# Optimization experiments

Measured on AMD Instinct MI355X. Metric: run time of the kernel, lower is better.

## Reference

```python
import jax, jax.numpy as jnp
import numpy as np
from jax import lax

# ---- module hyperparameters (from init_kwargs) ----
B = 8          # number of point clouds in the batch
NP = 4096      # points per cloud
C_IN = 64      # input feature channels
RATIO = 0.25   # fps ratio -> M_PER = 1024 centroids per cloud
R = 0.2        # ball-query radius
K = 64         # max_num_neighbors (hardcoded in the torch forward)
BIG = 1e10     # sentinel distance for out-of-radius pairs


def _fps(p, m):
    """Farthest point sampling on one cloud p:[Np,3] -> m local indices.
    Deterministic start at index 0 (torch_geometric uses a random start)."""
    mind = jnp.sum((p - p[0]) ** 2, axis=-1)  # [Np] dist^2 to first pick

    def step(mind, _):
        nxt = jnp.argmax(mind)
        d = jnp.sum((p - p[nxt]) ** 2, axis=-1)
        return jnp.minimum(mind, d), nxt

    _, rest = lax.scan(step, mind, None, length=m - 1)
    return jnp.concatenate([jnp.zeros((1,), rest.dtype), rest])  # [m]


def _ball_knn(p, s):
    """Radius query with neighbor cap: for each sampled point, the K nearest
    points within radius R (same cloud). p:[Np,3], s:[m] -> idx [m,K], mask [m,K].
    Note: every centroid contains itself (d=0), so each row has >=1 valid entry."""
    q = p[s]                                              # [m,3]
    d2 = jnp.sum((q[:, None, :] - p[None, :, :]) ** 2, axis=-1)  # [m,Np]
    dm = jnp.where(d2 <= R * R, d2, BIG)
    negv, idx = lax.top_k(-dm, K)                         # nearest-K within ball
    return idx, (-negv) < (BIG * 0.5)


def setup_inputs() -> dict:
    key = jax.random.key(0)
    k = jax.random.split(key, 6)
    x = jax.random.normal(k[0], (B * NP, C_IN), dtype=jnp.float32)
    pos = jax.random.uniform(k[1], (B * NP, 3), dtype=jnp.float32)  # unit cube
    batch = jnp.repeat(jnp.arange(B, dtype=jnp.int32), NP)

    def lin(kk, fi, fo):
        return jax.random.normal(kk, (fi, fo), dtype=jnp.float32) / np.float32(np.sqrt(fi))

    W1 = lin(k[2], C_IN + 3, 64); b1 = jnp.zeros((64,), jnp.float32)
    W2 = lin(k[3], 64, 64);       b2 = jnp.zeros((64,), jnp.float32)
    W3 = lin(k[4], 64, 128);      b3 = jnp.zeros((128,), jnp.float32)
    return dict(x=x, pos=pos, batch=batch, W1=W1, b1=b1, W2=W2, b2=b2,
                W3=W3, b3=b3, num_graphs=B)


def reference(x, pos, batch, W1, b1, W2, b2, W3, b3, num_graphs):
    Bn = int(num_graphs)
    N = pos.shape[0]
    Np = N // Bn
    m = int(Np * RATIO)

    posb = pos.reshape(Bn, Np, 3)
    sel = jax.vmap(lambda p: _fps(p, m))(posb)          # [B,m] local idx
    nbr, mask = jax.vmap(_ball_knn)(posb, sel)          # [B,m,K]

    offs = jnp.arange(Bn, dtype=sel.dtype) * Np
    sel_g = (sel + offs[:, None]).reshape(-1)           # [M] global centroid idx
    nbr_g = (nbr + offs[:, None, None]).reshape(Bn * m, K)
    maskf = mask.reshape(Bn * m, K)

    pos_s = pos[sel_g]                                  # [M,3]
    rel = pos[nbr_g] - pos_s[:, None, :]                # [M,K,3] pos_j - pos_i
    h = jnp.concatenate([x[nbr_g], rel], axis=-1)       # [M,K,C_IN+3]
    # PointNetConv local_nn (Linear-ReLU-Linear-ReLU-Linear), max aggregation
    h = jax.nn.relu(h @ W1 + b1)
    h = jax.nn.relu(h @ W2 + b2)
    h = h @ W3 + b3                                     # [M,K,128]
    h = jnp.where(maskf[:, :, None], h, jnp.float32(-1e30))
    x_out = jnp.max(h, axis=1)                          # [M,128]

    return x_out, pos_s, batch[sel_g]
```

## Files before the change

kernel.cpp:

```cpp
#include <hip/hip_runtime.h>
#include <math.h>

#define NB   8
#define NPTS 4096
#define MPER 1024
#define MTOT (NB*MPER)
#define CIN  64
#define KNN  64
#define CAP  512
#define R2D  0.04000000000000001

typedef unsigned int u32;
typedef unsigned long long u64;
using s16x8 = __attribute__((ext_vector_type(8))) short;
using f32x4 = __attribute__((ext_vector_type(4))) float;

__device__ __forceinline__ float d2f(float ax, float ay, float az,
                                     float bx, float by, float bz) {
    float dx = __fsub_rn(ax, bx);
    float dy = __fsub_rn(ay, by);
    float dz = __fsub_rn(az, bz);
    return __fadd_rn(__fadd_rn(__fmul_rn(dx, dx), __fmul_rn(dy, dy)),
                     __fmul_rn(dz, dz));
}

__device__ __forceinline__ unsigned short f2bf(float f) {
    u32 x = __float_as_uint(f);
    u32 r = (x + 0x7fffu + ((x >> 16) & 1u)) >> 16;
    return (unsigned short)r;
}
__device__ __forceinline__ u32 pk2(float a, float b) {
    return (u32)f2bf(a) | ((u32)f2bf(b) << 16);
}

__device__ __forceinline__ f32x4 mfma16(s16x8 a, s16x8 b, f32x4 c) {
    return __builtin_amdgcn_mfma_f32_16x16x32_bf16(a, b, c, 0, 0, 0);
}

__device__ __forceinline__ unsigned long long wave_max_u64_dpp(unsigned long long key)
{
#define DPPMAX(ctrl, rmask) do {                                                   \
        unsigned int lo_ = (unsigned int)key;                                      \
        unsigned int hi_ = (unsigned int)(key >> 32);                              \
        unsigned int plo = (unsigned int)__builtin_amdgcn_update_dpp(              \
            0, (int)lo_, ctrl, rmask, 0xf, false);                                 \
        unsigned int phi = (unsigned int)__builtin_amdgcn_update_dpp(              \
            0, (int)hi_, ctrl, rmask, 0xf, false);                                 \
        unsigned long long pk = ((unsigned long long)phi << 32) | plo;             \
        if (pk > key) key = pk;                                                    \
    } while (0)
    DPPMAX(0x111, 0xf);
    DPPMAX(0x112, 0xf);
    DPPMAX(0x114, 0xf);
    DPPMAX(0x118, 0xf);
    DPPMAX(0x142, 0xa);
    DPPMAX(0x143, 0xc);
#undef DPPMAX
    return key;
}

__global__ __launch_bounds__(256) void fps_kernel(const float* __restrict__ pos,
                                                  int* __restrict__ sel)
{
    const int b    = blockIdx.x;
    const int t    = threadIdx.x;
    const int lane = t & 63;
    const int wv   = t >> 6;
    const float* pb = pos + (size_t)b * NPTS * 3;

    __shared__ float lx[NPTS], ly[NPTS], lz[NPTS];
    __shared__ unsigned long long part[2][4];

    float px[16], py[16], pz[16], mind[16];
#pragma unroll
    for (int r = 0; r < 16; ++r) {
        int j = r * 256 + t;
        float x = pb[j * 3 + 0];
        float y = pb[j * 3 + 1];
        float z = pb[j * 3 + 2];
        px[r] = x; py[r] = y; pz[r] = z;
        mind[r] = 3.0e38f;
        lx[j] = x; ly[j] = y; lz[j] = z;
    }
    if (t == 0) sel[b * MPER + 0] = b * NPTS + 0;
    __syncthreads();

    float cx = lx[0], cy = ly[0], cz = lz[0];

    for (int it = 1; it < MPER; ++it) {
        float bv = -1.0f; int bi = 0;
#pragma unroll
        for (int r = 0; r < 16; ++r) {
            float d2 = d2f(px[r], py[r], pz[r], cx, cy, cz);
            float m = fminf(mind[r], d2);
            mind[r] = m;
            if (m > bv) { bv = m; bi = r * 256 + t; }
        }
        unsigned long long key =
            ((unsigned long long)__float_as_uint(bv) << 32) | (unsigned int)(~bi);
        key = wave_max_u64_dpp(key);

        const int p = it & 1;
        if (lane == 63) part[p][wv] = key;
        __syncthreads();

        unsigned long long k0 = part[p][0];
        unsigned long long k1 = part[p][1];
        unsigned long long k2 = part[p][2];
        unsigned long long k3 = part[p][3];
        unsigned long long ka = k0 > k1 ? k0 : k1;
        unsigned long long kb = k2 > k3 ? k2 : k3;
        unsigned long long km = ka > kb ? ka : kb;
        int pick = (int)(~(u32)km);

        cx = lx[pick]; cy = ly[pick]; cz = lz[pick];
        if (t == 0) sel[b * MPER + it] = b * NPTS + pick;
    }
}

__global__ __launch_bounds__(256) void ballq_kernel(
    const float* __restrict__ pos, const int* __restrict__ sel,
    int* __restrict__ nbr, int* __restrict__ cnt,
    float* __restrict__ out_pos, float* __restrict__ out_batch)
{
    __shared__ float cd[4][CAP];
    __shared__ int   ci[4][CAP];

    const int wv   = threadIdx.x >> 6;
    const int lane = threadIdx.x & 63;
    const int c    = blockIdx.x * 4 + wv;
    const int sg   = sel[c];
    const int b    = c >> 10;
    const int base = b * NPTS;
    const float* pb = pos + (size_t)base * 3;
    const float qx = pos[(size_t)sg * 3 + 0];
    const float qy = pos[(size_t)sg * 3 + 1];
    const float qz = pos[(size_t)sg * 3 + 2];

    int n = 0;
    for (int r0 = 0; r0 < NPTS; r0 += 64) {
        const int j = r0 + lane;
        float x = pb[j * 3 + 0], y = pb[j * 3 + 1], z = pb[j * 3 + 2];
        float d2 = d2f(x, y, z, qx, qy, qz);
        bool inside = ((double)d2 <= R2D);
        unsigned long long m = __ballot(inside);
        if (inside) {
            int myoff = n + __popcll(m & ((1ull << lane) - 1ull));
            if (myoff < CAP) { cd[wv][myoff] = d2; ci[wv][myoff] = j; }
        }
        n += __popcll(m);
    }
    n = min(n, CAP);
    __syncthreads();

    for (int i = lane; i < n; i += 64) {
        float d = cd[wv][i]; int id = ci[wv][i];
        int rank = 0;
        for (int j = 0; j < n; ++j) {
            float dj = cd[wv][j]; int ij = ci[wv][j];
            rank += (dj < d || (dj == d && ij < id)) ? 1 : 0;
        }
        if (rank < KNN) nbr[(size_t)c * KNN + rank] = base + id;
    }
    if (lane == 0) {
        cnt[c] = min(n, KNN);
        out_pos[c * 3 + 0] = qx;
        out_pos[c * 3 + 1] = qy;
        out_pos[c * 3 + 2] = qz;
        out_batch[c] = (float)b;
    }
}

#define W1T_U 6656
#define W2T_U 4608
#define W3T_U 9216
#define WTOT_U 20480

__global__ __launch_bounds__(256) void prep_weights(
    const float* __restrict__ W1, const float* __restrict__ W2,
    const float* __restrict__ W3, unsigned short* __restrict__ wsW)
{
    int i = blockIdx.x * 256 + threadIdx.x;
    if (i >= WTOT_U) return;
    float v;
    if (i < W1T_U) {
        int cr = i / 104, k = i - cr * 104;
        v = (k < 67) ? W1[k * 64 + cr] : 0.0f;
    } else if (i < W1T_U + W2T_U) {
        int j = i - W1T_U;
        int cr = j / 72, k = j - cr * 72;
        v = (k < 64) ? W2[k * 64 + cr] : 0.0f;
    } else {
        int j = i - (W1T_U + W2T_U);
        int cr = j / 72, k = j - cr * 72;
        v = (k < 64) ? W3[k * 128 + cr] : 0.0f;
    }
    wsW[i] = f2bf(v);
}

__global__ __launch_bounds__(256) void mlp_kernel(
    const float* __restrict__ x, const float* __restrict__ pos,
    const int* __restrict__ nbr, const int* __restrict__ cnt,
    const float* __restrict__ out_pos,
    const unsigned short* __restrict__ wsW,
    const float* __restrict__ b1, const float* __restrict__ b2,
    const float* __restrict__ b3,
    float* __restrict__ out_x)
{
    __shared__ __align__(16) unsigned short smA[6656];
    __shared__ __align__(16) unsigned short smW[WTOT_U];

    const int c = blockIdx.x;
    const int t = threadIdx.x;
    const int n = cnt[c];

    {
        const uint4* src = (const uint4*)wsW;
        uint4* dst = (uint4*)smW;
#pragma unroll
        for (int i = 0; i < 10; ++i) dst[t + 256 * i] = src[t + 256 * i];
    }

    {
        const int k = t >> 2, g = t & 3;
        const bool valid = k < n;
        const int nb = valid ? nbr[(size_t)c * KNN + k] : 0;
        const float* xr = x + (size_t)nb * CIN + g * 16;
        float4 f0, f1, f2, f3;
        if (valid) {
            f0 = *(const float4*)(xr + 0);
            f1 = *(const float4*)(xr + 4);
            f2 = *(const float4*)(xr + 8);
            f3 = *(const float4*)(xr + 12);
        } else {
            f0 = float4{0.f, 0.f, 0.f, 0.f};
            f1 = f0; f2 = f0; f3 = f0;
        }
        uint4 ua = { pk2(f0.x, f0.y), pk2(f0.z, f0.w), pk2(f1.x, f1.y), pk2(f1.z, f1.w) };
        uint4 ub = { pk2(f2.x, f2.y), pk2(f2.z, f2.w), pk2(f3.x, f3.y), pk2(f3.z, f3.w) };
        *(uint4*)&smA[k * 104 + g * 16 + 0] = ua;
        *(uint4*)&smA[k * 104 + g * 16 + 8] = ub;
        if (g == 0) {
            float r0 = 0.f, r1 = 0.f, r2 = 0.f;
            if (valid) {
                float q0 = out_pos[c * 3 + 0];
                float q1 = out_pos[c * 3 + 1];
                float q2 = out_pos[c * 3 + 2];
                r0 = __fsub_rn(pos[(size_t)nb * 3 + 0], q0);
                r1 = __fsub_rn(pos[(size_t)nb * 3 + 1], q1);
                r2 = __fsub_rn(pos[(size_t)nb * 3 + 2], q2);
            }
            uint4 uz = { 0u, 0u, 0u, 0u };
            uint4 ur = { pk2(r0, r1), (u32)f2bf(r2), 0u, 0u };
            *(uint4*)&smA[k * 104 + 64] = ur;
            *(uint4*)&smA[k * 104 + 72] = uz;
            *(uint4*)&smA[k * 104 + 80] = uz;
            *(uint4*)&smA[k * 104 + 88] = uz;
            *(uint4*)&smA[k * 104 + 96] = uz;
        }
    }
    __syncthreads();

    const int l  = t & 63;
    const int w  = t >> 6;
    const int lr = l & 15;
    const int kg = l >> 4;

    float bias1[4], bias2[4];
#pragma unroll
    for (int nt = 0; nt < 4; ++nt) {
        bias1[nt] = b1[nt * 16 + lr];
        bias2[nt] = b2[nt * 16 + lr];
    }

    const unsigned short* W1t = smW;
    const unsigned short* W2t = smW + W1T_U;
    const unsigned short* W3t = smW + W1T_U + W2T_U;
    unsigned short* H1 = smW;
    unsigned short* H2 = smA;

    f32x4 acc1[4];
#pragma unroll
    for (int nt = 0; nt < 4; ++nt) acc1[nt] = f32x4{0.f, 0.f, 0.f, 0.f};
    {
        const int ao = (w * 16 + lr) * 104 + kg * 8;
        const int bo = lr * 104 + kg * 8;
#pragma unroll
        for (int kc = 0; kc < 3; ++kc) {
            s16x8 af = *(const s16x8*)&smA[ao + kc * 32];
#pragma unroll
            for (int nt = 0; nt < 4; ++nt) {
                s16x8 bf = *(const s16x8*)&W1t[bo + nt * 1664 + kc * 32];
                acc1[nt] = mfma16(af, bf, acc1[nt]);
            }
        }
    }
    __syncthreads();
#pragma unroll
    for (int nt = 0; nt < 4; ++nt) {
        const int col = nt * 16 + lr;
#pragma unroll
        for (int r = 0; r < 4; ++r) {
            const int row = w * 16 + kg * 4 + r;
            float v = fmaxf(acc1[nt][r] + bias1[nt], 0.0f);
            H1[row * 72 + col] = f2bf(v);
        }
    }
    __syncthreads();

    f32x4 acc2[4];
#pragma unroll
    for (int nt = 0; nt < 4; ++nt) acc2[nt] = f32x4{0.f, 0.f, 0.f, 0.f};
    {
        const int ao = (w * 16 + lr) * 72 + kg * 8;
        const int bo = lr * 72 + kg * 8;
#pragma unroll
        for (int kc = 0; kc < 2; ++kc) {
            s16x8 af = *(const s16x8*)&H1[ao + kc * 32];
#pragma unroll
            for (int nt = 0; nt < 4; ++nt) {
                s16x8 bf = *(const s16x8*)&W2t[bo + nt * 1152 + kc * 32];
                acc2[nt] = mfma16(af, bf, acc2[nt]);
            }
        }
    }
#pragma unroll
    for (int nt = 0; nt < 4; ++nt) {
        const int col = nt * 16 + lr;
#pragma unroll
        for (int r = 0; r < 4; ++r) {
            const int row = w * 16 + kg * 4 + r;
            float v = fmaxf(acc2[nt][r] + bias2[nt], 0.0f);
            H2[row * 72 + col] = f2bf(v);
        }
    }
    __syncthreads();

    f32x4 acc3[8];
#pragma unroll
    for (int nt = 0; nt < 8; ++nt) acc3[nt] = f32x4{0.f, 0.f, 0.f, 0.f};
    {
        const int ao = (w * 16 + lr) * 72 + kg * 8;
        const int bo = lr * 72 + kg * 8;
#pragma unroll
        for (int kc = 0; kc < 2; ++kc) {
            s16x8 af = *(const s16x8*)&H2[ao + kc * 32];
#pragma unroll
            for (int nt = 0; nt < 8; ++nt) {
                s16x8 bf = *(const s16x8*)&W3t[bo + nt * 1152 + kc * 32];
                acc3[nt] = mfma16(af, bf, acc3[nt]);
            }
        }
    }

    float pm[8];
#pragma unroll
    for (int nt = 0; nt < 8; ++nt) pm[nt] = -1e30f;
#pragma unroll
    for (int r = 0; r < 4; ++r) {
        const int row = w * 16 + kg * 4 + r;
        if (row < n) {
#pragma unroll
            for (int nt = 0; nt < 8; ++nt) pm[nt] = fmaxf(pm[nt], acc3[nt][r]);
        }
    }
#pragma unroll
    for (int nt = 0; nt < 8; ++nt) {
        pm[nt] = fmaxf(pm[nt], __shfl_xor(pm[nt], 16));
        pm[nt] = fmaxf(pm[nt], __shfl_xor(pm[nt], 32));
    }
    __syncthreads();
    float* pbuf = (float*)smA;
    if (kg == 0) {
#pragma unroll
        for (int nt = 0; nt < 8; ++nt) pbuf[w * 128 + nt * 16 + lr] = pm[nt];
    }
    __syncthreads();
    if (t < 128) {
        float m = fmaxf(fmaxf(pbuf[t], pbuf[128 + t]),
                        fmaxf(pbuf[256 + t], pbuf[384 + t]));
        out_x[(size_t)c * 128 + t] = m + b3[t];
    }
}

extern "C" void kernel_launch(void* const* d_in, const int* in_sizes, int n_in,
                              void* d_out, int out_size, void* d_ws, size_t ws_size,
                              hipStream_t stream)
{
    const float* x   = (const float*)d_in[0];
    const float* pos = (const float*)d_in[1];
    const float* W1 = (const float*)d_in[3];
    const float* b1 = (const float*)d_in[4];
    const float* W2 = (const float*)d_in[5];
    const float* b2 = (const float*)d_in[6];
    const float* W3 = (const float*)d_in[7];
    const float* b3 = (const float*)d_in[8];

    float* out_x     = (float*)d_out;
    float* out_pos   = out_x + (size_t)MTOT * 128;
    float* out_batch = out_pos + (size_t)MTOT * 3;

    int* sel = (int*)d_ws;
    int* nbr = sel + MTOT;
    int* cnt = nbr + (size_t)MTOT * KNN;
    unsigned short* wsW = (unsigned short*)(cnt + MTOT);

    prep_weights<<<(WTOT_U + 255) / 256, 256, 0, stream>>>(W1, W2, W3, wsW);
    fps_kernel<<<NB, 256, 0, stream>>>(pos, sel);
    ballq_kernel<<<MTOT / 4, 256, 0, stream>>>(pos, sel, nbr, cnt, out_pos, out_batch);
    mlp_kernel<<<MTOT, 256, 0, stream>>>(x, pos, nbr, cnt, out_pos, wsW,
                                         b1, b2, b3, out_x);
}
```

Measured before the change: 767.3 us.

## Pack FPS distance math into v_pk f32 ops and replace barrier with tagged spin-wait

The FPS inner loop now computes distances for two points at a time with packed v_pk_add/v_pk_mul f32 instructions, halving the VALU instruction count for the distance update. The per-iteration __syncthreads is replaced by an iteration-tagged key in shared memory that each wave spin-reads until all four waves have published for the current step, removing the block barrier from the serial 1023-step chain. This relies on volatile LDS visibility and double-buffering with an 8-bit tag for correctness. The index encoding also changes from ~bi to 4095-bi so the tag fits.

After: 969.4 us. 26.3% more time.

```diff
diff --git a/kernel.cpp b/kernel.cpp
--- a/kernel.cpp
+++ b/kernel.cpp
@@ -12,6 +12,7 @@
 
 typedef unsigned int u32;
 typedef unsigned long long u64;
+typedef float v2f __attribute__((ext_vector_type(2)));
 using s16x8 = __attribute__((ext_vector_type(8))) short;
 using f32x4 = __attribute__((ext_vector_type(4))) float;
 
@@ -22,6 +23,17 @@
     float dz = __fsub_rn(az, bz);
     return __fadd_rn(__fadd_rn(__fmul_rn(dx, dx), __fmul_rn(dy, dy)),
                      __fmul_rn(dz, dz));
+}
+
+__device__ __forceinline__ v2f pk_add(v2f a, v2f b) {
+    v2f d;
+    asm("v_pk_add_f32 %0, %1, %2" : "=v"(d) : "v"(a), "v"(b));
+    return d;
+}
+__device__ __forceinline__ v2f pk_mul(v2f a, v2f b) {
+    v2f d;
+    asm("v_pk_mul_f32 %0, %1, %2" : "=v"(d) : "v"(a), "v"(b));
+    return d;
 }
 
 __device__ __forceinline__ unsigned short f2bf(float f) {
@@ -69,49 +81,69 @@
     const float* pb = pos + (size_t)b * NPTS * 3;
 
     __shared__ float lx[NPTS], ly[NPTS], lz[NPTS];
-    __shared__ unsigned long long part[2][4];
-
-    float px[16], py[16], pz[16], mind[16];
-#pragma unroll
-    for (int r = 0; r < 16; ++r) {
-        int j = r * 256 + t;
-        float x = pb[j * 3 + 0];
-        float y = pb[j * 3 + 1];
-        float z = pb[j * 3 + 2];
-        px[r] = x; py[r] = y; pz[r] = z;
-        mind[r] = 3.0e38f;
-        lx[j] = x; ly[j] = y; lz[j] = z;
-    }
+    __shared__ u64 skey[2][4];
+
+    v2f px[8], py[8], pz[8], mind[8];
+#pragma unroll
+    for (int pr = 0; pr < 8; ++pr) {
+        int j0 = (2 * pr + 0) * 256 + t;
+        int j1 = (2 * pr + 1) * 256 + t;
+        float x0 = pb[j0 * 3 + 0], y0 = pb[j0 * 3 + 1], z0 = pb[j0 * 3 + 2];
+        float x1 = pb[j1 * 3 + 0], y1 = pb[j1 * 3 + 1], z1 = pb[j1 * 3 + 2];
+        px[pr] = v2f{x0, x1}; py[pr] = v2f{y0, y1}; pz[pr] = v2f{z0, z1};
+        mind[pr] = v2f{3.0e38f, 3.0e38f};
+        lx[j0] = x0; ly[j0] = y0; lz[j0] = z0;
+        lx[j1] = x1; ly[j1] = y1; lz[j1] = z1;
+    }
+    if (t < 8) ((volatile u64*)&skey[0][0])[t] = 0ull;
     if (t == 0) sel[b * MPER + 0] = b * NPTS + 0;
     __syncthreads();
 
     float cx = lx[0], cy = ly[0], cz = lz[0];
+    volatile u64* vk = &skey[0][0];
 
     for (int it = 1; it < MPER; ++it) {
+        const v2f ncx = v2f{-cx, -cx};
+        const v2f ncy = v2f{-cy, -cy};
+        const v2f ncz = v2f{-cz, -cz};
+
         float bv = -1.0f; int bi = 0;
 #pragma unroll
-        for (int r = 0; r < 16; ++r) {
-            float d2 = d2f(px[r], py[r], pz[r], cx, cy, cz);
-            float m = fminf(mind[r], d2);
-            mind[r] = m;
-            if (m > bv) { bv = m; bi = r * 256 + t; }
-        }
-        unsigned long long key =
-            ((unsigned long long)__float_as_uint(bv) << 32) | (unsigned int)(~bi);
+        for (int pr = 0; pr < 8; ++pr) {
+            v2f dx = pk_add(px[pr], ncx);
+            v2f dy = pk_add(py[pr], ncy);
+            v2f dz = pk_add(pz[pr], ncz);
+            v2f s  = pk_add(pk_mul(dx, dx), pk_mul(dy, dy));
+            v2f d2 = pk_add(s, pk_mul(dz, dz));
+            float m0 = fminf(mind[pr].x, d2.x);
+            float m1 = fminf(mind[pr].y, d2.y);
+            mind[pr].x = m0; mind[pr].y = m1;
+            if (m0 > bv) { bv = m0; bi = (2 * pr + 0) * 256 + t; }
+            if (m1 > bv) { bv = m1; bi = (2 * pr + 1) * 256 + t; }
+        }
+
+        const u32 tag = (u32)it & 255u;
+        u64 key = ((u64)__float_as_uint(bv) << 32)
+                | (u64)((tag << 12) | (u32)(4095 - bi));
         key = wave_max_u64_dpp(key);
 
         const int p = it & 1;
-        if (lane == 63) part[p][wv] = key;
-        __syncthreads();
-
-        unsigned long long k0 = part[p][0];
-        unsigned long long k1 = part[p][1];
-        unsigned long long k2 = part[p][2];
-        unsigned long long k3 = part[p][3];
-        unsigned long long ka = k0 > k1 ? k0 : k1;
-        unsigned long long kb = k2 > k3 ? k2 : k3;
-        unsigned long long km = ka > kb ? ka : kb;
-        int pick = (int)(~(u32)km);
+        if (lane == 63) *((volatile u64*)&skey[p][wv]) = key;
+
+        u64 q0, q1, q2, q3;
+        for (;;) {
+            q0 = vk[p * 4 + 0]; q1 = vk[p * 4 + 1];
+            q2 = vk[p * 4 + 2]; q3 = vk[p * 4 + 3];
+            if (((((u32)q0 >> 12) & 255u) == tag) &&
+                ((((u32)q1 >> 12) & 255u) == tag) &&
+                ((((u32)q2 >> 12) & 255u) == tag) &&
+                ((((u32)q3 >> 12) & 255u) == tag)) break;
+        }
+
+        u64 ka = q0 > q1 ? q0 : q1;
+        u64 kb = q2 > q3 ? q2 : q3;
+        u64 km = ka > kb ? ka : kb;
+        int pick = 4095 - (int)((u32)km & 0xFFFu);
 
         cx = lx[pick]; cy = ly[pick]; cz = lz[pick];
         if (t == 0) sel[b * MPER + it] = b * NPTS + pick;
```
